# Optimization experiments

Measured on AMD Instinct MI355X. Metric: run time of the kernel, lower is better.

## Reference

```python
import jax, jax.numpy as jnp
import numpy as np

BOS_ID = 0
EOS_ID = 1


def setup_inputs() -> dict:
    key = jax.random.key(0)
    ks = jax.random.split(key, 16)
    B, L, F = 64, 200, 512
    H, E, A = 512, 512, 512
    V, T = 50257, 21
    D = E + F  # rnn input_dim
    s = lambda n: 1.0 / np.sqrt(n)
    ref = jax.random.randint(ks[0], (B, T), 2, V, dtype=jnp.int32)
    ref = ref.at[:, 0].set(BOS_ID).at[:, -1].set(EOS_ID)
    return {
        "encoder_output": jax.random.normal(ks[1], (B, L, F), jnp.float32),
        "decoder_init_hidden": jax.random.normal(ks[2], (1, B, H), jnp.float32),
        "encoding_mask": jnp.ones((B, L, 1), jnp.float32),
        "temp_seg": jax.random.uniform(ks[3], (B, 2), jnp.float32),
        "embed_table": jax.random.normal(ks[4], (V, E), jnp.float32) * 0.02,
        "W_ih": jax.random.normal(ks[5], (3 * H, D), jnp.float32) * s(D),
        "W_hh": jax.random.normal(ks[6], (3 * H, H), jnp.float32) * s(H),
        "b_ih": jnp.zeros((3 * H,), jnp.float32),
        "b_hh": jnp.zeros((3 * H,), jnp.float32),
        "Wa_enc": jax.random.normal(ks[7], (F, A), jnp.float32) * s(F),
        "Wa_h": jax.random.normal(ks[8], (H, A), jnp.float32) * s(H),
        "v_att": jax.random.normal(ks[9], (A,), jnp.float32) * s(A),
        "W_out": jax.random.normal(ks[10], (V, H), jnp.float32) * s(H),
        "b_out": jnp.zeros((V,), jnp.float32),
        "ref_caption": ref,
    }


def reference(encoder_output, decoder_init_hidden, encoding_mask, temp_seg,
              embed_table, W_ih, W_hh, b_ih, b_hh,
              Wa_enc, Wa_h, v_att, W_out, b_out, ref_caption):
    # Teacher-forced training forward of RNNSeqDecoder (GRU, 1 layer).
    B, T = ref_caption.shape
    V = embed_table.shape[0]
    enc_proj = jnp.einsum('blf,fa->bla', encoder_output, Wa_enc)  # precompute attn enc term
    mask = encoding_mask[..., 0]  # (B,L)
    h0 = decoder_init_hidden[0]   # (B,H)

    def step(h, word):
        emb = embed_table[word]                                        # (B,E)
        # additive attention over encoder states (masked)
        score = jnp.einsum('bla,a->bl', jnp.tanh(enc_proj + (h @ Wa_h)[:, None, :]), v_att)
        score = jnp.where(mask > 0, score, -1e9)
        attn = jax.nn.softmax(score, axis=1)
        ctx = jnp.einsum('bl,blf->bf', attn, encoder_output)           # (B,F)
        x = jnp.concatenate([emb, ctx], axis=1)                        # (B,E+F)
        # PyTorch GRU cell
        gi = x @ W_ih.T + b_ih
        gh = h @ W_hh.T + b_hh
        i_r, i_z, i_n = jnp.split(gi, 3, axis=1)
        h_r, h_z, h_n = jnp.split(gh, 3, axis=1)
        r = jax.nn.sigmoid(i_r + h_r)
        z = jax.nn.sigmoid(i_z + h_z)
        n = jnp.tanh(i_n + r * h_n)
        h_new = (1.0 - z) * n + z * h
        logp = jax.nn.log_softmax(h_new @ W_out.T + b_out, axis=1)     # (B,V)
        return h_new, logp

    _, logps = jax.lax.scan(step, h0, ref_caption[:, :-1].T)           # (T-1,B,V)
    first = jnp.zeros((B, 1, V), logps.dtype)  # BOS_ID == 0, matches torch.zeros(...) + BOS_ID
    caption_prob = jnp.concatenate([first, jnp.swapaxes(logps, 0, 1)], axis=1)  # (B,T,V)
    return caption_prob
```

## Files before the change

### kernel.cpp

```cpp
#include <hip/hip_runtime.h>
#include <stdint.h>
#include <stddef.h>

#define B_ 64
#define L_ 200
#define F_ 512
#define H_ 512
#define A_ 512
#define E_ 512
#define V_ 50257
#define PADV 50304
#define T_ 21
#define D_ 1024
#define NBLK_LOG 786
#define BH (B_ * H_)
#define BD (B_ * D_)
#define NROW 1280

typedef __attribute__((ext_vector_type(8))) short short8;
typedef __attribute__((ext_vector_type(4))) float f32x4;

__device__ __forceinline__ unsigned short f2b(float f) {
  unsigned int u = __builtin_bit_cast(unsigned int, f);
  u += 0x7FFFu + ((u >> 16) & 1u);
  return (unsigned short)(u >> 16);
}
__device__ __forceinline__ float b2f(unsigned short s) {
  unsigned int u = ((unsigned int)s) << 16;
  return __builtin_bit_cast(float, u);
}
__device__ __forceinline__ f32x4 mfma16(short8 a, short8 b, f32x4 c) {
  return __builtin_amdgcn_mfma_f32_16x16x32_bf16(a, b, c, 0, 0, 0);
}
__device__ __forceinline__ int hsoff(int b, int j) {
  return (((b >> 4) * 16 + (j >> 5)) * 64 + (((j >> 3) & 3) * 16 + (b & 15))) * 8 + (j & 7);
}
__device__ __forceinline__ int xoff(int b, int k) {
  return (((b >> 4) * 32 + (k >> 5)) * 64 + (((k >> 3) & 3) * 16 + (b & 15))) * 8 + (k & 7);
}


__device__ void cvt_dev(const float* __restrict__ src, unsigned short* __restrict__ dst,
                        int n4, int vbid, int nblk) {
  int i = vbid * 256 + threadIdx.x;
  int stride = nblk * 256;
  const float4* s4 = (const float4*)src;
  ushort4* d4 = (ushort4*)dst;
  for (; i < n4; i += stride) {
    float4 v = s4[i];
    ushort4 o;
    o.x = f2b(v.x); o.y = f2b(v.y); o.z = f2b(v.z); o.w = f2b(v.w);
    d4[i] = o;
  }
}

__device__ void wfrag_dev(const float* __restrict__ src, unsigned short* __restrict__ dst,
                          int K, int rt) {
  int r15 = threadIdx.x & 15;
  int row = rt * 16 + r15;
  int nch = K >> 3;
  int kpw = K >> 5;
  for (int kc = threadIdx.x >> 4; kc < nch; kc += 16) {
    const float4* s = (const float4*)(src + (size_t)row * K + kc * 8);
    float4 x = s[0], y = s[1];
    short8 o;
    o[0] = f2b(x.x); o[1] = f2b(x.y); o[2] = f2b(x.z); o[3] = f2b(x.w);
    o[4] = f2b(y.x); o[5] = f2b(y.y); o[6] = f2b(y.z); o[7] = f2b(y.w);
    *(short8*)(dst + ((size_t)(rt * kpw + (kc >> 2)) * 64 + ((kc & 3) * 16 + r15)) * 8) = o;
  }
}

__global__ __launch_bounds__(256) void k_setupA(const float* __restrict__ Wout, unsigned short* __restrict__ Wb,
                                                const float* __restrict__ enc, unsigned short* __restrict__ encb,
                                                const float* __restrict__ Wih, unsigned short* __restrict__ Wfih,
                                                const float* __restrict__ Whh, unsigned short* __restrict__ Wfhh,
                                                const float* __restrict__ Waenc, unsigned short* __restrict__ WaTb,
                                                const float* __restrict__ Wah, float* __restrict__ WahT32,
                                                const float* __restrict__ dih, unsigned short* __restrict__ hsAll,
                                                const int* __restrict__ ref, const float* __restrict__ et,
                                                unsigned short* __restrict__ xAll) {
  __shared__ float tile[64][65];
  int bid = blockIdx.x;
  int tid = threadIdx.x;
  if (bid < 4096) {
    cvt_dev(Wout, Wb, V_ * H_ / 4, bid, 4096);
  } else if (bid < 6144) {
    cvt_dev(enc, encb, B_ * L_ * F_ / 4, bid - 4096, 2048);
  } else if (bid < 6240) {
    wfrag_dev(Wih, Wfih, 1024, bid - 6144);
  } else if (bid < 6336) {
    wfrag_dev(Whh, Wfhh, 512, bid - 6240);
  } else if (bid < 6400) {
    int q = bid - 6336;
    int cb = (q & 7) * 64, rb = (q >> 3) * 64;
    int tx = tid & 63, ty = tid >> 6;
#pragma unroll
    for (int i = 0; i < 16; ++i) {
      int r = ty * 16 + i;
      tile[r][tx] = Waenc[(size_t)(rb + r) * 512 + cb + tx];
    }
    __syncthreads();
#pragma unroll
    for (int i = 0; i < 16; ++i) {
      int c = ty * 16 + i;
      WaTb[(size_t)(cb + c) * 512 + rb + tx] = f2b(tile[tx][c]);
    }
  } else if (bid < 6464) {
    int q = bid - 6400;
    int cb = (q & 7) * 64, rb = (q >> 3) * 64;
    int tx = tid & 63, ty = tid >> 6;
#pragma unroll
    for (int i = 0; i < 16; ++i) {
      int r = ty * 16 + i;
      tile[r][tx] = Wah[(size_t)(rb + r) * 512 + cb + tx];
    }
    __syncthreads();
#pragma unroll
    for (int i = 0; i < 16; ++i) {
      int c = ty * 16 + i;
      WahT32[(size_t)(cb + c) * 512 + rb + tx] = tile[tx][c];
    }
  } else if (bid < 6528) {
    int b = bid - 6464;
    for (int j = tid; j < H_; j += 256)
      hsAll[hsoff(b, j)] = f2b(dih[(size_t)b * H_ + j]);
  } else {
    int q = bid - 6528;
    int b = q & 63, tp = q >> 6;
    if (tid < 64) {
      int word = ref[b * T_ + tp];
      const float* er = et + (size_t)word * E_;
      unsigned short* dst = xAll + (size_t)tp * BD;
      int c = tid;
      const float4* s = (const float4*)(er + c * 8);
      float4 x = s[0], y = s[1];
      short8 o;
      o[0] = f2b(x.x); o[1] = f2b(x.y); o[2] = f2b(x.z); o[3] = f2b(x.w);
      o[4] = f2b(y.x); o[5] = f2b(y.y); o[6] = f2b(y.z); o[7] = f2b(y.w);
      *(short8*)(dst + xoff(b, c * 8)) = o;
    }
  }
}

__global__ __launch_bounds__(256) void k_setupB(const float* __restrict__ WahT32,
                                                unsigned short* __restrict__ Wahf,
                                                const unsigned short* __restrict__ encb,
                                                const unsigned short* __restrict__ WaTb,
                                                unsigned short* __restrict__ epb) {
  __shared__ unsigned short al[32768];
  int bid = blockIdx.x;
  int tid = threadIdx.x;
  if (bid < 32) {
    wfrag_dev(WahT32, Wahf, 512, bid);
    return;
  }
  size_t rowbase = (size_t)(bid - 32) * 64;
  for (int idx = tid; idx < 4096; idx += 256) {
    int row = idx >> 6, seg = idx & 63;
    unsigned char* dp = (unsigned char*)al + row * 1024 + ((seg * 16) ^ ((row & 7) << 4));
    *(short8*)dp = *(const short8*)(encb + (rowbase + row) * F_ + seg * 8);
  }
  __syncthreads();
  int w = tid >> 6, lane = tid & 63, ln15 = lane & 15, g = lane >> 4;
  int sw = (ln15 & 7) << 4;
  const unsigned char* alb = (const unsigned char*)al;
  int mrow = w * 16 + ln15;
  for (int nt = 0; nt < 32; ++nt) {
    f32x4 acc = {0.f, 0.f, 0.f, 0.f};
    const unsigned short* brow = WaTb + (size_t)(nt * 16 + ln15) * F_ + 8 * g;
#pragma unroll 4
    for (int kk = 0; kk < 16; ++kk) {
      short8 bf = *(const short8*)(brow + kk * 32);
      short8 af = *(const short8*)(alb + mrow * 1024 + ((kk * 64 + 16 * g) ^ sw));
      acc = mfma16(af, bf, acc);
    }
#pragma unroll
    for (int r = 0; r < 4; ++r) {
      size_t m = rowbase + w * 16 + 4 * g + r;
      epb[m * A_ + nt * 16 + ln15] = f2b(acc[r]);
    }
  }
}


__global__ __launch_bounds__(256) void k_hwgh(const unsigned short* __restrict__ Wahf,
                                              const unsigned short* __restrict__ Wfhh,
                                              const unsigned short* __restrict__ hs,
                                              float* __restrict__ hw,
                                              float* __restrict__ ghG) {
  int blk = blockIdx.x;
  int w = threadIdx.x >> 6, lane = threadIdx.x & 63;
  int ln15 = lane & 15, g = lane >> 4;
  if (blk < 32) {
    f32x4 acc = {0.f, 0.f, 0.f, 0.f};
#pragma unroll 4
    for (int kk = 0; kk < 16; ++kk) {
      short8 av = *(const short8*)(Wahf + (((size_t)blk * 16 + kk) * 64 + lane) * 8);
      short8 hv = *(const short8*)(hs + (((size_t)w * 16 + kk) * 64 + lane) * 8);
      acc = mfma16(av, hv, acc);
    }
#pragma unroll
    for (int r = 0; r < 4; ++r) {
      int a = blk * 16 + 4 * g + r;
      int b = w * 16 + ln15;
      hw[(size_t)b * 512 + a] = acc[r];
    }
  } else {
    int jt = blk - 32;
    f32x4 acc = {0.f, 0.f, 0.f, 0.f};
#pragma unroll
    for (int kk = 0; kk < 16; ++kk) {
      short8 wv = *(const short8*)(Wfhh + (((size_t)jt * 16 + kk) * 64 + lane) * 8);
      short8 hv = *(const short8*)(hs + (((size_t)w * 16 + kk) * 64 + lane) * 8);
      acc = mfma16(wv, hv, acc);
    }
#pragma unroll
    for (int r = 0; r < 4; ++r) {
      int j = jt * 16 + 4 * g + r;
      int b = w * 16 + ln15;
      ghG[(size_t)j * B_ + b] = acc[r];
    }
  }
}


__global__ __launch_bounds__(1024) void k_attB(const float* __restrict__ mask,
                                               const float* __restrict__ vatt,
                                               const unsigned short* __restrict__ encb,
                                               const unsigned short* __restrict__ epb,
                                               const float* __restrict__ hw,
                                               unsigned short* __restrict__ xplane) {
  __shared__ float sm[208];
  __shared__ float ctxp[16][F_];
  __shared__ float ctxF[F_];
  int b = blockIdx.x;
  int tid = threadIdx.x;
  int w = tid >> 6, lane = tid & 63;
  float hwv[8], vv[8];
  {
    const float4* hp = (const float4*)(hw + (size_t)b * 512 + lane * 8);
    const float4* vp = (const float4*)(vatt + lane * 8);
    float4 h0 = hp[0], h1 = hp[1], v0 = vp[0], v1 = vp[1];
    hwv[0] = h0.x; hwv[1] = h0.y; hwv[2] = h0.z; hwv[3] = h0.w;
    hwv[4] = h1.x; hwv[5] = h1.y; hwv[6] = h1.z; hwv[7] = h1.w;
    vv[0] = v0.x; vv[1] = v0.y; vv[2] = v0.z; vv[3] = v0.w;
    vv[4] = v1.x; vv[5] = v1.y; vv[6] = v1.z; vv[7] = v1.w;
  }
  for (int l = w; l < L_; l += 16) {
    short8 ev = *(const short8*)(epb + ((size_t)(b * L_ + l)) * 512 + lane * 8);
    float p = 0.f;
#pragma unroll
    for (int j = 0; j < 8; ++j) {
      float x = b2f((unsigned short)ev[j]) + hwv[j];
      float e2 = __expf(x + x);
      p = fmaf(1.f - 2.f / (e2 + 1.f), vv[j], p);
    }
    for (int o = 1; o < 64; o <<= 1) p += __shfl_xor(p, o);
    if (lane == 0) {
      float mk = mask[b * L_ + l];
      sm[l] = (mk > 0.f) ? p : -1e9f;
    }
  }
  __syncthreads();
  if (tid < 64) {
    float m = -1e30f;
    for (int l = tid; l < L_; l += 64) m = fmaxf(m, sm[l]);
    for (int o = 1; o < 64; o <<= 1) m = fmaxf(m, __shfl_xor(m, o));
    float s = 0.f;
    for (int l = tid; l < L_; l += 64) s += __expf(sm[l] - m);
    for (int o = 1; o < 64; o <<= 1) s += __shfl_xor(s, o);
    float inv = 1.f / s;
    for (int l = tid; l < L_; l += 64) sm[l] = __expf(sm[l] - m) * inv;
  }
  __syncthreads();
  float c[8] = {0.f, 0.f, 0.f, 0.f, 0.f, 0.f, 0.f, 0.f};
  for (int l = w; l < L_; l += 16) {
    float wgt = sm[l];
    short8 ev = *(const short8*)(encb + ((size_t)(b * L_ + l)) * 512 + lane * 8);
#pragma unroll
    for (int j = 0; j < 8; ++j) c[j] = fmaf(wgt, b2f((unsigned short)ev[j]), c[j]);
  }
#pragma unroll
  for (int j = 0; j < 8; ++j) ctxp[w][lane * 8 + j] = c[j];
  __syncthreads();
  if (tid < 512) {
    float s = 0.f;
#pragma unroll
    for (int q = 0; q < 16; ++q) s += ctxp[q][tid];
    ctxF[tid] = s;
  }
  __syncthreads();
  if (tid < 64) {
    short8 o;
#pragma unroll
    for (int j = 0; j < 8; ++j) o[j] = f2b(ctxF[tid * 8 + j]);
    *(short8*)(xplane + xoff(b, E_ + tid * 8)) = o;
  }
}


__global__ __launch_bounds__(256) void k_stepB(const unsigned short* __restrict__ Wfih,
                                               const float* __restrict__ bih,
                                               const float* __restrict__ bhh,
                                               const unsigned short* __restrict__ xplane,
                                               const float* __restrict__ ghG,
                                               const float* __restrict__ hBold,
                                               unsigned short* __restrict__ hsnew,
                                               float* __restrict__ hBnew) {
  int bx = blockIdx.x;
  int w = threadIdx.x >> 6, lane = threadIdx.x & 63;
  int ln15 = lane & 15, g = lane >> 4;
  f32x4 z4 = {0.f, 0.f, 0.f, 0.f};
  f32x4 aIr = z4, aIz = z4, aIn = z4;
#pragma unroll 2
  for (int kk = 0; kk < 32; ++kk) {
    short8 xv = *(const short8*)(xplane + (((size_t)w * 32 + kk) * 64 + lane) * 8);
    aIr = mfma16(*(const short8*)(Wfih + (((size_t)(0 * 32 + bx) * 32 + kk) * 64 + lane) * 8), xv, aIr);
    aIz = mfma16(*(const short8*)(Wfih + (((size_t)(32 + bx) * 32 + kk) * 64 + lane) * 8), xv, aIz);
    aIn = mfma16(*(const short8*)(Wfih + (((size_t)(64 + bx) * 32 + kk) * 64 + lane) * 8), xv, aIn);
  }
  int jb = bx * 16;
#pragma unroll
  for (int r = 0; r < 4; ++r) {
    int j = jb + 4 * g + r;
    int b = w * 16 + ln15;
    float ir = aIr[r] + bih[j];
    float iz = aIz[r] + bih[512 + j];
    float in_ = aIn[r] + bih[1024 + j];
    float hrv = ghG[(size_t)j * B_ + b] + bhh[j];
    float hzv = ghG[(size_t)(512 + j) * B_ + b] + bhh[512 + j];
    float hnv = ghG[(size_t)(1024 + j) * B_ + b] + bhh[1024 + j];
    float rg = 1.f / (1.f + __expf(-(ir + hrv)));
    float zg = 1.f / (1.f + __expf(-(iz + hzv)));
    float e2 = __expf(2.f * (in_ + rg * hnv));
    float ng = 1.f - 2.f / (e2 + 1.f);
    float ho = hBold[(size_t)b * H_ + j];
    float hv = (1.f - zg) * ng + zg * ho;
    hBnew[(size_t)b * H_ + j] = hv;
    hsnew[hsoff(b, j)] = f2b(hv);
  }
}


__global__ __launch_bounds__(256) void k_blog(const unsigned short* __restrict__ Wb,
                                              const float* __restrict__ bout,
                                              const unsigned short* __restrict__ hsAll,
                                              float* __restrict__ out,
                                              unsigned short* __restrict__ lws, int mode) {
  __shared__ float tile[2][64][68];
  int tid = threadIdx.x;
  int w = tid >> 6, lane = tid & 63, ln15 = lane & 15, g = lane >> 4;
  int vcol = blockIdx.x * 64 + w * 16 + ln15;
  bool vok = vcol < V_;
  int vr = vok ? vcol : (V_ - 1);
  const unsigned short* brow = Wb + (size_t)vr * H_ + 8 * g;
  short8 wb[16];
#pragma unroll
  for (int kk = 0; kk < 16; ++kk) wb[kk] = *(const short8*)(brow + kk * 32);
  float bo = bout[vr];
  int row = tid >> 2, seg = tid & 3;

  for (int t = 0; t < T_ - 1; ++t) {
    const unsigned short* hp = hsAll + (size_t)(t + 1) * BH;
    int buf = t & 1;
    __builtin_amdgcn_s_setprio(1);
#pragma unroll
    for (int mp = 0; mp < 2; ++mp) {
      f32x4 z4 = {0.f, 0.f, 0.f, 0.f};
      f32x4 acc0 = z4, acc1 = z4;
#pragma unroll
      for (int kk = 0; kk < 16; ++kk) {
        short8 a0 = *(const short8*)(hp + (((mp * 2 + 0) * 16 + kk) * 64 + lane) * 8);
        short8 a1 = *(const short8*)(hp + (((mp * 2 + 1) * 16 + kk) * 64 + lane) * 8);
        acc0 = mfma16(a0, wb[kk], acc0);
        acc1 = mfma16(a1, wb[kk], acc1);
      }
#pragma unroll
      for (int r = 0; r < 4; ++r) {
        int bi0 = (mp * 2 + 0) * 16 + 4 * g + r;
        int bi1 = (mp * 2 + 1) * 16 + 4 * g + r;
        tile[buf][bi0][w * 16 + ln15] = vok ? acc0[r] + bo : -1e30f;
        tile[buf][bi1][w * 16 + ln15] = vok ? acc1[r] + bo : -1e30f;
      }
    }
    __builtin_amdgcn_s_setprio(0);
    __syncthreads();
    float v[16];
#pragma unroll
    for (int q = 0; q < 4; ++q) {
      float4 fv = *(const float4*)&tile[buf][row][seg * 16 + q * 4];
      v[q * 4 + 0] = fv.x; v[q * 4 + 1] = fv.y; v[q * 4 + 2] = fv.z; v[q * 4 + 3] = fv.w;
    }
    int cb = blockIdx.x * 64 + seg * 16;
    if (mode == 1) {
      unsigned short* orow = lws + ((size_t)t * 64 + row) * PADV + cb;
      short8 o0, o1;
#pragma unroll
      for (int i = 0; i < 8; ++i) { o0[i] = f2b(v[i]); o1[i] = f2b(v[8 + i]); }
      *(short8*)orow = o0;
      *(short8*)(orow + 8) = o1;
    } else {
      float* orow = out + ((size_t)row * T_ + (t + 1)) * V_ + cb;
      if (cb + 16 <= V_) {
#pragma unroll
        for (int q = 0; q < 4; ++q)
          *(float4*)(orow + q * 4) = make_float4(v[q * 4], v[q * 4 + 1], v[q * 4 + 2], v[q * 4 + 3]);
      } else {
        for (int i = 0; i < 16; ++i)
          if (cb + i < V_) orow[i] = v[i];
      }
    }
  }
}


__global__ __launch_bounds__(512) void k_lsefin(const unsigned short* __restrict__ lws,
                                                float* __restrict__ out) {
  __shared__ unsigned short srow[PADV];
  __shared__ float lm[512], ls[512];
  __shared__ float lvs;
  int bid = blockIdx.x;
  int tid = threadIdx.x;
  if (bid >= NROW) {
    int b = bid - NROW;
    float* o = out + (size_t)b * T_ * V_;
    float4 z = make_float4(0.f, 0.f, 0.f, 0.f);
    for (int i = tid; i < 12564; i += 512) *(float4*)(o + i * 4) = z;
    if (tid == 0) o[50256] = 0.f;
    return;
  }
  int rho = bid;
  int tp = rho >> 6, b = rho & 63;
  const unsigned short* src = lws + (size_t)(tp * 64 + b) * PADV;
  float* o = out + ((size_t)b * T_ + (tp + 1)) * V_;
  float m = -1e30f, s = 0.f;
  for (int i = tid; i < PADV / 8; i += 512) {
    short8 sv = *(const short8*)(src + i * 8);
    *(short8*)(srow + i * 8) = sv;
    float x0 = b2f((unsigned short)sv[0]), x1 = b2f((unsigned short)sv[1]);
    float x2 = b2f((unsigned short)sv[2]), x3 = b2f((unsigned short)sv[3]);
    float x4 = b2f((unsigned short)sv[4]), x5 = b2f((unsigned short)sv[5]);
    float x6 = b2f((unsigned short)sv[6]), x7 = b2f((unsigned short)sv[7]);
    float cm = fmaxf(fmaxf(fmaxf(x0, x1), fmaxf(x2, x3)), fmaxf(fmaxf(x4, x5), fmaxf(x6, x7)));
    float cs = __expf(x0 - cm) + __expf(x1 - cm) + __expf(x2 - cm) + __expf(x3 - cm) +
               __expf(x4 - cm) + __expf(x5 - cm) + __expf(x6 - cm) + __expf(x7 - cm);
    float nm = fmaxf(m, cm);
    s = s * __expf(m - nm) + cs * __expf(cm - nm);
    m = nm;
  }
  lm[tid] = m; ls[tid] = s;
  __syncthreads();
  for (int o2 = 256; o2 > 0; o2 >>= 1) {
    if (tid < o2) {
      float m2 = lm[tid + o2], s2 = ls[tid + o2];
      float nm = fmaxf(lm[tid], m2);
      ls[tid] = ls[tid] * __expf(lm[tid] - nm) + s2 * __expf(m2 - nm);
      lm[tid] = nm;
    }
    __syncthreads();
  }
  if (tid == 0) lvs = lm[0] + logf(ls[0]);
  __syncthreads();
  float Lv = lvs;
  for (int i = tid; i < 6282; i += 512) {
    short8 sv = *(const short8*)(srow + i * 8);
    float4 v0, v1;
    v0.x = b2f((unsigned short)sv[0]) - Lv; v0.y = b2f((unsigned short)sv[1]) - Lv;
    v0.z = b2f((unsigned short)sv[2]) - Lv; v0.w = b2f((unsigned short)sv[3]) - Lv;
    v1.x = b2f((unsigned short)sv[4]) - Lv; v1.y = b2f((unsigned short)sv[5]) - Lv;
    v1.z = b2f((unsigned short)sv[6]) - Lv; v1.w = b2f((unsigned short)sv[7]) - Lv;
    *(float4*)(o + i * 8) = v0;
    *(float4*)(o + i * 8 + 4) = v1;
  }
  if (tid == 0) o[50256] = b2f(srow[50256]) - Lv;
}

__global__ __launch_bounds__(256) void k_lsefin0(float* __restrict__ out) {
  __shared__ float lm[256], ls[256];
  __shared__ float lvs;
  int bid = blockIdx.x;
  int tid = threadIdx.x;
  if (bid >= NROW) {
    int b = bid - NROW;
    float* o = out + (size_t)b * T_ * V_;
    for (int v = tid; v < V_; v += 256) o[v] = 0.f;
    return;
  }
  int rho = bid;
  int tp = rho >> 6, b = rho & 63;
  float* o = out + ((size_t)b * T_ + (tp + 1)) * V_;
  float m = -1e30f, s = 0.f;
  for (int v = tid; v < V_; v += 256) {
    float x = o[v];
    float nm = fmaxf(m, x);
    s = s * __expf(m - nm) + __expf(x - nm);
    m = nm;
  }
  lm[tid] = m; ls[tid] = s;
  __syncthreads();
  for (int o2 = 128; o2 > 0; o2 >>= 1) {
    if (tid < o2) {
      float m2 = lm[tid + o2], s2 = ls[tid + o2];
      float nm = fmaxf(lm[tid], m2);
      ls[tid] = ls[tid] * __expf(lm[tid] - nm) + s2 * __expf(m2 - nm);
      lm[tid] = nm;
    }
    __syncthreads();
  }
  if (tid == 0) lvs = lm[0] + logf(ls[0]);
  __syncthreads();
  float Lv = lvs;
  for (int v = tid; v < V_; v += 256) o[v] -= Lv;
}


extern "C" void kernel_launch(void* const* d_in, const int* in_sizes, int n_in,
                              void* d_out, int out_size, void* d_ws, size_t ws_size,
                              hipStream_t stream) {
  const float* enc   = (const float*)d_in[0];
  const float* dih   = (const float*)d_in[1];
  const float* mask  = (const float*)d_in[2];
  const float* et    = (const float*)d_in[4];
  const float* Wih   = (const float*)d_in[5];
  const float* Whh   = (const float*)d_in[6];
  const float* bih   = (const float*)d_in[7];
  const float* bhh   = (const float*)d_in[8];
  const float* Waenc = (const float*)d_in[9];
  const float* Wah   = (const float*)d_in[10];
  const float* vatt  = (const float*)d_in[11];
  const float* Wout  = (const float*)d_in[12];
  const float* bout  = (const float*)d_in[13];
  const int*   ref   = (const int*)d_in[14];
  float* out = (float*)d_out;

  char* w = (char*)d_ws;
  size_t o = 0;
  unsigned short* Wb    = (unsigned short*)(w + o); o += (size_t)V_ * H_ * 2;
  unsigned short* Wfih  = (unsigned short*)(w + o); o += (size_t)1536 * 1024 * 2;
  unsigned short* Wfhh  = (unsigned short*)(w + o); o += (size_t)1536 * 512 * 2;
  unsigned short* WaTb  = (unsigned short*)(w + o); o += (size_t)512 * 512 * 2;
  unsigned short* Wahf  = (unsigned short*)(w + o); o += (size_t)512 * 512 * 2;
  float* WahT32 = (float*)(w + o); o += (size_t)512 * 512 * 4;
  unsigned short* encb  = (unsigned short*)(w + o); o += (size_t)B_ * L_ * F_ * 2;
  unsigned short* epb   = (unsigned short*)(w + o); o += (size_t)B_ * L_ * A_ * 2;
  unsigned short* xAll  = (unsigned short*)(w + o); o += (size_t)20 * BD * 2;
  unsigned short* hsAll = (unsigned short*)(w + o); o += (size_t)T_ * BH * 2;
  float* hBAll = (float*)(w + o); o += (size_t)T_ * BH * 4;
  float* ghG   = (float*)(w + o); o += (size_t)1536 * B_ * 4;
  float* hw    = (float*)(w + o); o += (size_t)B_ * A_ * 4 + 256;
  unsigned short* lws = (unsigned short*)(w + o);
  size_t need = o + (size_t)NROW * PADV * 2;
  int mode = (ws_size >= need) ? 1 : 0;

  k_setupA<<<7808, 256, 0, stream>>>(Wout, Wb, enc, encb, Wih, Wfih, Whh, Wfhh,
                                     Waenc, WaTb, Wah, WahT32, dih, hsAll, ref, et, xAll);
  k_setupB<<<232, 256, 0, stream>>>(WahT32, Wahf, encb, WaTb, epb);

  for (int t = 0; t < T_ - 1; ++t) {
    const float* hB_t = (t == 0) ? dih : (hBAll + (size_t)t * BH);
    float* hB_n = hBAll + (size_t)(t + 1) * BH;
    const unsigned short* hs_t = hsAll + (size_t)t * BH;
    unsigned short* hs_n = hsAll + (size_t)(t + 1) * BH;
    unsigned short* xp = xAll + (size_t)t * BD;
    k_hwgh<<<128, 256, 0, stream>>>(Wahf, Wfhh, hs_t, hw, ghG);
    k_attB<<<64, 1024, 0, stream>>>(mask, vatt, encb, epb, hw, xp);
    k_stepB<<<32, 256, 0, stream>>>(Wfih, bih, bhh, xp, ghG, hB_t, hs_n, hB_n);
  }
  k_blog<<<NBLK_LOG, 256, 0, stream>>>(Wb, bout, hsAll, out, lws, mode);
  if (mode == 1) k_lsefin<<<NROW + 64, 512, 0, stream>>>(lws, out);
  else k_lsefin0<<<NROW + 64, 256, 0, stream>>>(out);
}
```

Before: 1.320 ms.

## Split logits kernel into 32-column blocks with waves sharing batch halves

The output-projection kernel now covers 32 vocab columns per block instead of 64, doubling the grid. Each pair of waves splits the 64 batch rows between them rather than one wave handling all rows for its 16 columns, so each wave issues half the MFMAs per step. The shared staging tile now holds bf16 instead of fp32, which shrinks LDS use and makes the mode-1 store a direct short8 copy. The trade-off is that each W_out slice is loaded into registers by two waves, and in mode 0 the logits are rounded to bf16 before being written.

```diff
diff --git a/kernel.cpp b/kernel.cpp
--- a/kernel.cpp
+++ b/kernel.cpp
@@ -12,7 +12,7 @@
 #define PADV 50304
 #define T_ 21
 #define D_ 1024
-#define NBLK_LOG 786
+#define NBLK32 1572
 #define BH (B_ * H_)
 #define BD (B_ * D_)
 #define NROW 1280
@@ -347,10 +347,11 @@
                                               const unsigned short* __restrict__ hsAll,
                                               float* __restrict__ out,
                                               unsigned short* __restrict__ lws, int mode) {
-  __shared__ float tile[2][64][68];
+  __shared__ unsigned short tile[2][64][40];
   int tid = threadIdx.x;
   int w = tid >> 6, lane = tid & 63, ln15 = lane & 15, g = lane >> 4;
-  int vcol = blockIdx.x * 64 + w * 16 + ln15;
+  int ch = w & 1, mh = w >> 1;
+  int vcol = blockIdx.x * 32 + ch * 16 + ln15;
   bool vok = vcol < V_;
   int vr = vok ? vcol : (V_ - 1);
   const unsigned short* brow = Wb + (size_t)vr * H_ + 8 * g;
@@ -364,50 +365,38 @@
     const unsigned short* hp = hsAll + (size_t)(t + 1) * BH;
     int buf = t & 1;
     __builtin_amdgcn_s_setprio(1);
-#pragma unroll
-    for (int mp = 0; mp < 2; ++mp) {
-      f32x4 z4 = {0.f, 0.f, 0.f, 0.f};
-      f32x4 acc0 = z4, acc1 = z4;
-#pragma unroll
-      for (int kk = 0; kk < 16; ++kk) {
-        short8 a0 = *(const short8*)(hp + (((mp * 2 + 0) * 16 + kk) * 64 + lane) * 8);
-        short8 a1 = *(const short8*)(hp + (((mp * 2 + 1) * 16 + kk) * 64 + lane) * 8);
-        acc0 = mfma16(a0, wb[kk], acc0);
-        acc1 = mfma16(a1, wb[kk], acc1);
-      }
-#pragma unroll
-      for (int r = 0; r < 4; ++r) {
-        int bi0 = (mp * 2 + 0) * 16 + 4 * g + r;
-        int bi1 = (mp * 2 + 1) * 16 + 4 * g + r;
-        tile[buf][bi0][w * 16 + ln15] = vok ? acc0[r] + bo : -1e30f;
-        tile[buf][bi1][w * 16 + ln15] = vok ? acc1[r] + bo : -1e30f;
-      }
+    f32x4 z4 = {0.f, 0.f, 0.f, 0.f};
+    f32x4 acc0 = z4, acc1 = z4;
+#pragma unroll
+    for (int kk = 0; kk < 16; ++kk) {
+      short8 a0 = *(const short8*)(hp + (((mh * 2 + 0) * 16 + kk) * 64 + lane) * 8);
+      short8 a1 = *(const short8*)(hp + (((mh * 2 + 1) * 16 + kk) * 64 + lane) * 8);
+      acc0 = mfma16(a0, wb[kk], acc0);
+      acc1 = mfma16(a1, wb[kk], acc1);
     }
     __builtin_amdgcn_s_setprio(0);
+#pragma unroll
+    for (int r = 0; r < 4; ++r) {
+      int bi0 = (mh * 2 + 0) * 16 + 4 * g + r;
+      int bi1 = (mh * 2 + 1) * 16 + 4 * g + r;
+      int col = ch * 16 + ln15;
+      tile[buf][bi0][col] = vok ? f2b(acc0[r] + bo) : f2b(-1e30f);
+      tile[buf][bi1][col] = vok ? f2b(acc1[r] + bo) : f2b(-1e30f);
+    }
     __syncthreads();
-    float v[16];
-#pragma unroll
-    for (int q = 0; q < 4; ++q) {
-      float4 fv = *(const float4*)&tile[buf][row][seg * 16 + q * 4];
-      v[q * 4 + 0] = fv.x; v[q * 4 + 1] = fv.y; v[q * 4 + 2] = fv.z; v[q * 4 + 3] = fv.w;
-    }
-    int cb = blockIdx.x * 64 + seg * 16;
+    int cb = blockIdx.x * 32 + seg * 8;
     if (mode == 1) {
-      unsigned short* orow = lws + ((size_t)t * 64 + row) * PADV + cb;
-      short8 o0, o1;
-#pragma unroll
-      for (int i = 0; i < 8; ++i) { o0[i] = f2b(v[i]); o1[i] = f2b(v[8 + i]); }
-      *(short8*)orow = o0;
-      *(short8*)(orow + 8) = o1;
+      short8 sv = *(const short8*)&tile[buf][row][seg * 8];
+      *(short8*)(lws + ((size_t)t * 64 + row) * PADV + cb) = sv;
     } else {
+      short8 sv = *(const short8*)&tile[buf][row][seg * 8];
       float* orow = out + ((size_t)row * T_ + (t + 1)) * V_ + cb;
-      if (cb + 16 <= V_) {
-#pragma unroll
-        for (int q = 0; q < 4; ++q)
-          *(float4*)(orow + q * 4) = make_float4(v[q * 4], v[q * 4 + 1], v[q * 4 + 2], v[q * 4 + 3]);
+      if (cb + 8 <= V_) {
+#pragma unroll
+        for (int i = 0; i < 8; ++i) orow[i] = b2f((unsigned short)sv[i]);
       } else {
-        for (int i = 0; i < 16; ++i)
-          if (cb + i < V_) orow[i] = v[i];
+        for (int i = 0; i < 8; ++i)
+          if (cb + i < V_) orow[i] = b2f((unsigned short)sv[i]);
       }
     }
   }
@@ -566,7 +555,7 @@
     k_attB<<<64, 1024, 0, stream>>>(mask, vatt, encb, epb, hw, xp);
     k_stepB<<<32, 256, 0, stream>>>(Wfih, bih, bhh, xp, ghG, hB_t, hs_n, hB_n);
   }
-  k_blog<<<NBLK_LOG, 256, 0, stream>>>(Wb, bout, hsAll, out, lws, mode);
+  k_blog<<<NBLK32, 256, 0, stream>>>(Wb, bout, hsAll, out, lws, mode);
   if (mode == 1) k_lsefin<<<NROW + 64, 512, 0, stream>>>(lws, out);
   else k_lsefin0<<<NROW + 64, 256, 0, stream>>>(out);
 }
```

Result: no change. 1.304 ms (median of 2 runs) (-1.3%).
